# Kernel tuning notes

Measured on AMD Instinct MI355X. Metric: run time of the kernel, lower is better.

The kernel has to match this reference:

```python
import math
import jax, jax.numpy as jnp
import numpy as np

NUM_HEADS = 16
D_MODEL = 1024
D_HEAD = 64
D_SEQ = 2048
NUM_LAYERS = 24
BATCH = 2


def setup_inputs() -> dict:
    key = jax.random.key(0)
    ks = jax.random.split(key, 10)
    s = math.sqrt(0.02)
    residual = jax.random.normal(ks[0], (BATCH, D_SEQ, D_MODEL), dtype=jnp.float32)
    W_Q = jax.random.normal(ks[1], (NUM_HEADS, D_MODEL, D_HEAD), dtype=jnp.float32) * s
    W_K = jax.random.normal(ks[2], (NUM_HEADS, D_MODEL, D_HEAD), dtype=jnp.float32) * s
    W_V = jax.random.normal(ks[3], (NUM_HEADS, D_MODEL, D_HEAD), dtype=jnp.float32) * s
    W_O = jax.random.normal(ks[4], (NUM_HEADS * D_HEAD, D_MODEL), dtype=jnp.float32) * s
    W_O = W_O / math.sqrt(NUM_LAYERS)
    b_Q = jax.random.normal(ks[5], (NUM_HEADS, D_HEAD), dtype=jnp.float32) * s
    b_K = jax.random.normal(ks[6], (NUM_HEADS, D_HEAD), dtype=jnp.float32) * s
    b_V = jax.random.normal(ks[7], (NUM_HEADS, D_HEAD), dtype=jnp.float32) * s
    b_O = jax.random.normal(ks[8], (D_MODEL,), dtype=jnp.float32) * s
    return dict(residual=residual, W_Q=W_Q, W_K=W_K, W_V=W_V, W_O=W_O,
                b_Q=b_Q, b_K=b_K, b_V=b_V, b_O=b_O)


def reference(residual, W_Q, W_K, W_V, W_O, b_Q, b_K, b_V, b_O):
    # residual: [b, s, m]; W_{Q,K,V}: [h, m, d]; b_{Q,K,V}: [h, d]
    Q = jnp.einsum('hmd,bsm->bshd', W_Q, residual) + b_Q
    K = jnp.einsum('hmd,bsm->bshd', W_K, residual) + b_K
    V = jnp.einsum('hmd,bsm->bshd', W_V, residual) + b_V
    # full causal score matrix [b, h, s_q, s_k], masked with -inf above diagonal
    QK = jnp.einsum('bqhd,bkhd->bhqk', Q, K)
    seq = residual.shape[1]
    causal = jnp.triu(jnp.ones((seq, seq), dtype=bool), k=1)  # True above diag
    QK_masked = jnp.where(causal, -jnp.inf, QK)
    soft = jax.nn.softmax(QK_masked / math.sqrt(D_HEAD), axis=-1)
    attn = jnp.einsum('bhqk,bkhd->bqhd', soft, V)  # [b, s, h, d]
    multi_head = attn.reshape(attn.shape[0], attn.shape[1], NUM_HEADS * D_HEAD)
    return jnp.einsum('em,bqe->bqm', W_O, multi_head) + b_O
```

## Files before the change

kernel.cpp:

```cpp
#include <hip/hip_runtime.h>
#include <stdint.h>

typedef unsigned short u16;
typedef unsigned long long u64;
typedef _Float16 f16;
typedef __attribute__((ext_vector_type(8))) _Float16 f16x8;
typedef __attribute__((ext_vector_type(4))) float f32x4;
typedef __attribute__((ext_vector_type(16))) float f32x16;
typedef __attribute__((ext_vector_type(4))) unsigned short u16x4;
typedef __attribute__((ext_vector_type(8))) unsigned short u16x8;

#define NHEADS 16
#define DMODEL 1024
#define DHEAD 64
#define SEQ 2048
#define NBATCH 2
#define MROWS (NBATCH * SEQ)
#define NQKV 3072
#define SCQ 0.18033688011112042f

__device__ __forceinline__ u16 f2h(float x) {
  union { f16 h; u16 u; } v;
  v.h = (f16)x;
  return v.u;
}

__device__ __forceinline__ unsigned pk2u(float x, float y) {
  typedef __fp16 fp16x2 __attribute__((ext_vector_type(2)));
  fp16x2 h = __builtin_amdgcn_cvt_pkrtz(x, y);
  union { fp16x2 h; unsigned u; } v; v.h = h;
  return v.u;
}

__device__ __forceinline__ f16x8 mkfrag(unsigned w0, unsigned w1, unsigned w2, unsigned w3) {
  union { unsigned u[4]; f16x8 f; } t;
  t.u[0] = w0; t.u[1] = w1; t.u[2] = w2; t.u[3] = w3;
  return t.f;
}

__device__ __forceinline__ f16x8 vfrag(const char* row, int sz, int F, int hib8) {
  union { u64 u[2]; f16x8 f; } t;
  t.u[0] = *(const u64*)(row + (((2 * F) ^ sz) << 4) + hib8);
  t.u[1] = *(const u64*)(row + (((2 * F + 1) ^ sz) << 4) + hib8);
  return t.f;
}

__device__ __forceinline__ void gload_lds16(const void* g, void* l) {
  __builtin_amdgcn_global_load_lds(
      (const __attribute__((address_space(1))) void*)g,
      (__attribute__((address_space(3))) void*)l, 16, 0, 0);
}

__global__ __launch_bounds__(256) void prep_kernel(
    const float* __restrict__ X,
    const float* __restrict__ WQ, const float* __restrict__ WK,
    const float* __restrict__ WV, const float* __restrict__ WO,
    u16* __restrict__ Xh, u16* __restrict__ Wqkv, u16* __restrict__ Wo) {
  __shared__ u16 lt[64][72];
  int blk = blockIdx.x;
  if (blk < 2048) {
    int i = blk * 256 + threadIdx.x;
    const f32x4* xv = (const f32x4*)(X + (size_t)i * 8);
    f32x4 a = xv[0], b = xv[1];
    u16x8 o;
    o[0] = f2h(a[0]); o[1] = f2h(a[1]); o[2] = f2h(a[2]); o[3] = f2h(a[3]);
    o[4] = f2h(b[0]); o[5] = f2h(b[1]); o[6] = f2h(b[2]); o[7] = f2h(b[3]);
    *(u16x8*)(Xh + (size_t)i * 8) = o;
  } else if (blk < 2816) {
    int bb = blk - 2048;
    int mt = bb & 15, hh = (bb >> 4) & 15, qkv = bb >> 8;
    const float* W = (qkv == 0) ? WQ : (qkv == 1) ? WK : WV;
    int m_in = threadIdx.x >> 2, dq = threadIdx.x & 3;
    const f32x4* sp4 = (const f32x4*)(W + (size_t)hh * (DMODEL * DHEAD) +
                                      (size_t)(mt * 64 + m_in) * DHEAD + dq * 16);
#pragma unroll
    for (int v4 = 0; v4 < 4; ++v4) {
      f32x4 a = sp4[v4];
#pragma unroll
      for (int j = 0; j < 4; ++j) lt[dq * 16 + v4 * 4 + j][m_in] = f2h(a[j]);
    }
    __syncthreads();
    int d_in = threadIdx.x >> 2, mq = threadIdx.x & 3;
    size_t orow = ((size_t)(qkv * 1024 + hh * 64 + d_in)) * DMODEL + mt * 64 + mq * 16;
    u16x8 o0, o1;
#pragma unroll
    for (int j = 0; j < 8; ++j) {
      o0[j] = lt[d_in][mq * 16 + j];
      o1[j] = lt[d_in][mq * 16 + 8 + j];
    }
    *(u16x8*)(Wqkv + orow) = o0;
    *(u16x8*)(Wqkv + orow + 8) = o1;
  } else {
    int bb = blk - 2816;
    int mt = bb & 15, et = bb >> 4;
    int e_in = threadIdx.x >> 2, mq = threadIdx.x & 3;
    const f32x4* sp4 = (const f32x4*)(WO + (size_t)(et * 64 + e_in) * DMODEL + mt * 64 + mq * 16);
#pragma unroll
    for (int v4 = 0; v4 < 4; ++v4) {
      f32x4 a = sp4[v4];
#pragma unroll
      for (int j = 0; j < 4; ++j) lt[mq * 16 + v4 * 4 + j][e_in] = f2h(a[j]);
    }
    __syncthreads();
    int m_in = threadIdx.x >> 2, eq = threadIdx.x & 3;
    size_t orow = (size_t)(mt * 64 + m_in) * DMODEL + et * 64 + eq * 16;
    u16x8 o0, o1;
#pragma unroll
    for (int j = 0; j < 8; ++j) {
      o0[j] = lt[m_in][eq * 16 + j];
      o1[j] = lt[m_in][eq * 16 + 8 + j];
    }
    *(u16x8*)(Wo + orow) = o0;
    *(u16x8*)(Wo + orow + 8) = o1;
  }
}

__global__ __launch_bounds__(256, 2) void gemm_qkv(
    const u16* __restrict__ A, const u16* __restrict__ Bt,
    const float* __restrict__ bq, const float* __restrict__ bk, const float* __restrict__ bv,
    u16* __restrict__ Qo, u16* __restrict__ Ko, u16* __restrict__ Vto) {
  __shared__ u16 lds[2][8192];
  const int tid = threadIdx.x;
  const int wid = tid >> 6, lane = tid & 63, lr = lane & 15, lg = lane >> 4;
  const int wr = wid >> 1, wc = wid & 1;
  const int brow = blockIdx.y * 128, bcol = blockIdx.x * 128;

  f32x4 acc[4][4];
#pragma unroll
  for (int i = 0; i < 4; ++i)
#pragma unroll
    for (int j = 0; j < 4; ++j) acc[i][j] = (f32x4){0.f, 0.f, 0.f, 0.f};

#define STAGE(buf, kt)                                                               \
  {                                                                                  \
    _Pragma("unroll") for (int i = 0; i < 2; ++i) {                                  \
      int idx = tid + i * 256;                                                       \
      gload_lds16(A + (size_t)(brow + (idx >> 2)) * 1024 + (kt) * 32 + (idx & 3) * 8,\
                  (char*)&lds[buf][0] + (wid * 64 + i * 256) * 16);                  \
    }                                                                                \
    _Pragma("unroll") for (int i = 0; i < 2; ++i) {                                  \
      int idx = tid + i * 256;                                                       \
      gload_lds16(Bt + (size_t)(bcol + (idx >> 2)) * 1024 + (kt) * 32 + (idx & 3) * 8,\
                  (char*)&lds[buf][4096] + (wid * 64 + i * 256) * 16);               \
    }                                                                                \
  }

  STAGE(0, 0);
  __syncthreads();
  int cur = 0;
  for (int kt = 0; kt < 32; ++kt) {
    if (kt + 1 < 32) STAGE(cur ^ 1, kt + 1);
    const u16* Ab = &lds[cur][0];
    const u16* Bb = &lds[cur][4096];
    f16x8 a[4], b[4];
#pragma unroll
    for (int ar = 0; ar < 4; ++ar)
      a[ar] = *(const f16x8*)(Ab + (wr * 64 + ar * 16 + lr) * 32 + lg * 8);
#pragma unroll
    for (int bc = 0; bc < 4; ++bc)
      b[bc] = *(const f16x8*)(Bb + (wc * 64 + bc * 16 + lr) * 32 + lg * 8);
#pragma unroll
    for (int ar = 0; ar < 4; ++ar)
#pragma unroll
      for (int bc = 0; bc < 4; ++bc)
        acc[ar][bc] = __builtin_amdgcn_mfma_f32_16x16x32_f16(a[ar], b[bc], acc[ar][bc], 0, 0, 0);
    __syncthreads();
    cur ^= 1;
  }

#pragma unroll
  for (int ar = 0; ar < 4; ++ar) {
    int row0 = brow + wr * 64 + ar * 16 + lg * 4;
    int bb = row0 >> 11, s0 = row0 & 2047;
#pragma unroll
    for (int bc = 0; bc < 4; ++bc) {
      int n = bcol + wc * 64 + bc * 16 + lr;
      int qkv = n >> 10, hd = n & 1023, h = hd >> 6, d = hd & 63;
      float bias = ((qkv == 0) ? bq : (qkv == 1) ? bk : bv)[hd];
      if (qkv < 2) {
        u16* dst = qkv ? Ko : Qo;
        float sc = qkv ? 1.f : SCQ;
        size_t base = ((size_t)(bb * NHEADS + h) * SEQ + s0) * DHEAD + d;
#pragma unroll
        for (int r = 0; r < 4; ++r)
          dst[base + (size_t)r * DHEAD] = f2h((acc[ar][bc][r] + bias) * sc);
      } else {
        u16x4 o;
        o[0] = f2h(acc[ar][bc][0] + bias);
        o[1] = f2h(acc[ar][bc][1] + bias);
        o[2] = f2h(acc[ar][bc][2] + bias);
        o[3] = f2h(acc[ar][bc][3] + bias);
        *(u16x4*)(Vto + ((size_t)(bb * NHEADS + h) * DHEAD + d) * SEQ + s0) = o;
      }
    }
  }
}

__global__ __launch_bounds__(256, 2) void gemm_out(
    const u16* __restrict__ A, const u16* __restrict__ Bt,
    const float* __restrict__ bo, float* __restrict__ Co) {
  __shared__ u16 lds[2][8192];
  const int tid = threadIdx.x;
  const int wid = tid >> 6, lane = tid & 63, lr = lane & 15, lg = lane >> 4;
  const int wr = wid >> 1, wc = wid & 1;
  const int brow = blockIdx.y * 128, bcol = blockIdx.x * 128;

  f32x4 acc[4][4];
#pragma unroll
  for (int i = 0; i < 4; ++i)
#pragma unroll
    for (int j = 0; j < 4; ++j) acc[i][j] = (f32x4){0.f, 0.f, 0.f, 0.f};

  STAGE(0, 0);
  __syncthreads();
  int cur = 0;
  for (int kt = 0; kt < 32; ++kt) {
    if (kt + 1 < 32) STAGE(cur ^ 1, kt + 1);
    const u16* Ab = &lds[cur][0];
    const u16* Bb = &lds[cur][4096];
    f16x8 a[4], b[4];
#pragma unroll
    for (int ar = 0; ar < 4; ++ar)
      a[ar] = *(const f16x8*)(Ab + (wr * 64 + ar * 16 + lr) * 32 + lg * 8);
#pragma unroll
    for (int bc = 0; bc < 4; ++bc)
      b[bc] = *(const f16x8*)(Bb + (wc * 64 + bc * 16 + lr) * 32 + lg * 8);
#pragma unroll
    for (int ar = 0; ar < 4; ++ar)
#pragma unroll
      for (int bc = 0; bc < 4; ++bc)
        acc[ar][bc] = __builtin_amdgcn_mfma_f32_16x16x32_f16(a[ar], b[bc], acc[ar][bc], 0, 0, 0);
    __syncthreads();
    cur ^= 1;
  }
#undef STAGE

#pragma unroll
  for (int ar = 0; ar < 4; ++ar) {
    int row0 = brow + wr * 64 + ar * 16 + lg * 4;
#pragma unroll
    for (int bc = 0; bc < 4; ++bc) {
      int n = bcol + wc * 64 + bc * 16 + lr;
      float bias = bo[n];
#pragma unroll
      for (int r = 0; r < 4; ++r)
        Co[(size_t)(row0 + r) * DMODEL + n] = acc[ar][bc][r] + bias;
    }
  }
}

__global__ __launch_bounds__(128, 2) void attn_kernel(
    const u16* __restrict__ Q, const u16* __restrict__ K,
    const u16* __restrict__ Vt, u16* __restrict__ MH) {
  __shared__ char sh8[32768];
  const int tid = threadIdx.x, wid = tid >> 6, lane = tid & 63;
  const int l31 = lane & 31, hi = lane >> 5;
  const int bid = blockIdx.x;
  const int x = bid & 7, r = bid >> 3;
  const int bh = x + 8 * (r & 3);
  const int t = 31 - (r >> 2);
  const int h = bh & 15, b = bh >> 4;
  const u16* Qb = Q + (size_t)bh * (SEQ * DHEAD);
  const u16* Kb = K + (size_t)bh * (SEQ * DHEAD);
  const u16* Vb = Vt + (size_t)bh * (DHEAD * SEQ);

#pragma unroll
  for (int i = 0; i < 4; ++i) {
    int idx = tid + i * 128, row = idx >> 3;
    int sseg = (idx & 7) ^ ((row ^ (row >> 3)) & 7);
    gload_lds16(Qb + (size_t)(t * 64 + row) * DHEAD + sseg * 8, sh8 + 8192 + idx * 16);
    gload_lds16(Kb + (size_t)row * DHEAD + sseg * 8, sh8 + idx * 16);
    gload_lds16(Vb + (size_t)row * SEQ + sseg * 8, sh8 + 16384 + idx * 16);
  }
  __syncthreads();

  f16x8 qf0, qf1, qf2, qf3;
  {
    int row = (wid << 5) + l31;
    int swz = ((row ^ (row >> 3)) & 7) << 4;
    const char* qb = sh8 + 8192 + row * 128;
    qf0 = *(const f16x8*)(qb + ((hi * 16 + 0)  ^ swz));
    qf1 = *(const f16x8*)(qb + ((hi * 16 + 32) ^ swz));
    qf2 = *(const f16x8*)(qb + ((hi * 16 + 64) ^ swz));
    qf3 = *(const f16x8*)(qb + ((hi * 16 + 96) ^ swz));
  }
  __syncthreads();

  f32x16 acc0, acc1;
#pragma unroll
  for (int z = 0; z < 16; ++z) { acc0[z] = 0.f; acc1[z] = 0.f; }
  float m = -1e30f, l = 0.f;
  const int qa = t * 64 + (wid << 5) + l31;

  const int sw0 = (l31 ^ (l31 >> 3)) & 7;
  const int kz0 = sw0 << 4;
  const int r32 = 32 + l31;
  const int sw1 = (r32 ^ (r32 >> 3)) & 7;
  const int kz1 = sw1 << 4;
  const int hib = hi * 16;
  const int hib8 = hi * 8;

  for (int kt = 0; kt <= t; ++kt) {
    if (kt < t) {
      const int kb_n = ((kt + 1) & 1) ? 8192 : 0;
      const int vb_n = ((kt + 1) & 1) ? 24576 : 16384;
#pragma unroll
      for (int i = 0; i < 4; ++i) {
        int idx = tid + i * 128, rw = idx >> 3;
        int sseg = (idx & 7) ^ ((rw ^ (rw >> 3)) & 7);
        gload_lds16(Kb + (size_t)((kt + 1) * 64 + rw) * DHEAD + sseg * 8, sh8 + kb_n + idx * 16);
        gload_lds16(Vb + (size_t)rw * SEQ + (kt + 1) * 64 + sseg * 8, sh8 + vb_n + idx * 16);
      }
    }
    const char* kbuf = sh8 + ((kt & 1) ? 8192 : 0);
    const char* vbuf = sh8 + ((kt & 1) ? 24576 : 16384);

    f32x16 s0, s1;
#pragma unroll
    for (int z = 0; z < 16; ++z) { s0[z] = 0.f; s1[z] = 0.f; }
    {
      const char* kb0 = kbuf + l31 * 128;
      const char* kb1 = kbuf + r32 * 128;
      f16x8 kf;
      __builtin_amdgcn_s_setprio(1);
      kf = *(const f16x8*)(kb0 + ((hib + 0)  ^ kz0)); s0 = __builtin_amdgcn_mfma_f32_32x32x16_f16(kf, qf0, s0, 0, 0, 0);
      kf = *(const f16x8*)(kb0 + ((hib + 32) ^ kz0)); s0 = __builtin_amdgcn_mfma_f32_32x32x16_f16(kf, qf1, s0, 0, 0, 0);
      kf = *(const f16x8*)(kb0 + ((hib + 64) ^ kz0)); s0 = __builtin_amdgcn_mfma_f32_32x32x16_f16(kf, qf2, s0, 0, 0, 0);
      kf = *(const f16x8*)(kb0 + ((hib + 96) ^ kz0)); s0 = __builtin_amdgcn_mfma_f32_32x32x16_f16(kf, qf3, s0, 0, 0, 0);
      kf = *(const f16x8*)(kb1 + ((hib + 0)  ^ kz1)); s1 = __builtin_amdgcn_mfma_f32_32x32x16_f16(kf, qf0, s1, 0, 0, 0);
      kf = *(const f16x8*)(kb1 + ((hib + 32) ^ kz1)); s1 = __builtin_amdgcn_mfma_f32_32x32x16_f16(kf, qf1, s1, 0, 0, 0);
      kf = *(const f16x8*)(kb1 + ((hib + 64) ^ kz1)); s1 = __builtin_amdgcn_mfma_f32_32x32x16_f16(kf, qf2, s1, 0, 0, 0);
      kf = *(const f16x8*)(kb1 + ((hib + 96) ^ kz1)); s1 = __builtin_amdgcn_mfma_f32_32x32x16_f16(kf, qf3, s1, 0, 0, 0);
      __builtin_amdgcn_s_setprio(0);
    }

    if (kt == t) {
#pragma unroll
      for (int rr = 0; rr < 16; ++rr) {
        int k0 = kt * 64 + (rr & 3) + 8 * (rr >> 2) + 4 * hi;
        if (k0 > qa) s0[rr] = -1e30f;
        if (k0 + 32 > qa) s1[rr] = -1e30f;
      }
    }

    float tm = s0[0];
#pragma unroll
    for (int rr = 1; rr < 16; ++rr) tm = fmaxf(tm, s0[rr]);
#pragma unroll
    for (int rr = 0; rr < 16; ++rr) tm = fmaxf(tm, s1[rr]);
    tm = fmaxf(tm, __shfl_xor(tm, 32));

    if (!__all(tm <= m + 8.f)) {
      float m2 = fmaxf(m, tm);
      float al = exp2f(m - m2);
      m = m2;
      l *= al;
#pragma unroll
      for (int rr = 0; rr < 16; ++rr) {
        int qp = (rr & 3) + 8 * (rr >> 2) + 4 * hi;
        float af = __shfl(al, qp);
        acc0[rr] *= af;
        acc1[rr] *= af;
      }
    }

    float rs = 0.f;
#pragma unroll
    for (int rr = 0; rr < 16; ++rr) { s0[rr] = exp2f(s0[rr] - m); rs += s0[rr]; }
#pragma unroll
    for (int rr = 0; rr < 16; ++rr) { s1[rr] = exp2f(s1[rr] - m); rs += s1[rr]; }
    rs += __shfl_xor(rs, 32);
    l += rs;

    f16x8 pa0 = mkfrag(pk2u(s0[0],  s0[1]),  pk2u(s0[2],  s0[3]),
                       pk2u(s0[4],  s0[5]),  pk2u(s0[6],  s0[7]));
    f16x8 pa1 = mkfrag(pk2u(s0[8],  s0[9]),  pk2u(s0[10], s0[11]),
                       pk2u(s0[12], s0[13]), pk2u(s0[14], s0[15]));
    f16x8 pa2 = mkfrag(pk2u(s1[0],  s1[1]),  pk2u(s1[2],  s1[3]),
                       pk2u(s1[4],  s1[5]),  pk2u(s1[6],  s1[7]));
    f16x8 pa3 = mkfrag(pk2u(s1[8],  s1[9]),  pk2u(s1[10], s1[11]),
                       pk2u(s1[12], s1[13]), pk2u(s1[14], s1[15]));

    {
      const char* vr0 = vbuf + l31 * 128;
      const char* vr1 = vbuf + r32 * 128;
      __builtin_amdgcn_s_setprio(1);
      acc0 = __builtin_amdgcn_mfma_f32_32x32x16_f16(pa0, vfrag(vr0, sw0, 0, hib8), acc0, 0, 0, 0);
      acc0 = __builtin_amdgcn_mfma_f32_32x32x16_f16(pa1, vfrag(vr0, sw0, 1, hib8), acc0, 0, 0, 0);
      acc0 = __builtin_amdgcn_mfma_f32_32x32x16_f16(pa2, vfrag(vr0, sw0, 2, hib8), acc0, 0, 0, 0);
      acc0 = __builtin_amdgcn_mfma_f32_32x32x16_f16(pa3, vfrag(vr0, sw0, 3, hib8), acc0, 0, 0, 0);
      acc1 = __builtin_amdgcn_mfma_f32_32x32x16_f16(pa0, vfrag(vr1, sw1, 0, hib8), acc1, 0, 0, 0);
      acc1 = __builtin_amdgcn_mfma_f32_32x32x16_f16(pa1, vfrag(vr1, sw1, 1, hib8), acc1, 0, 0, 0);
      acc1 = __builtin_amdgcn_mfma_f32_32x32x16_f16(pa2, vfrag(vr1, sw1, 2, hib8), acc1, 0, 0, 0);
      acc1 = __builtin_amdgcn_mfma_f32_32x32x16_f16(pa3, vfrag(vr1, sw1, 3, hib8), acc1, 0, 0, 0);
      __builtin_amdgcn_s_setprio(0);
    }

    __syncthreads();
  }

#pragma unroll
  for (int rr = 0; rr < 16; ++rr) {
    int qp = (rr & 3) + 8 * (rr >> 2) + 4 * hi;
    float ls = __shfl(l, qp);
    int qrow = t * 64 + (wid << 5) + qp;
    size_t base = ((size_t)(b * SEQ) + qrow) * DMODEL + h * DHEAD;
    MH[base + l31]      = f2h(acc0[rr] / ls);
    MH[base + 32 + l31] = f2h(acc1[rr] / ls);
  }
}

extern "C" void kernel_launch(void* const* d_in, const int* in_sizes, int n_in,
                              void* d_out, int out_size, void* d_ws, size_t ws_size,
                              hipStream_t stream) {
  const float* residual = (const float*)d_in[0];
  const float* WQ = (const float*)d_in[1];
  const float* WK = (const float*)d_in[2];
  const float* WV = (const float*)d_in[3];
  const float* WO = (const float*)d_in[4];
  const float* bQ = (const float*)d_in[5];
  const float* bK = (const float*)d_in[6];
  const float* bV = (const float*)d_in[7];
  const float* bO = (const float*)d_in[8];
  float* out = (float*)d_out;

  char* w = (char*)d_ws;
  u16* Xh   = (u16*)(w);
  u16* Wqkv = (u16*)(w + ((size_t)8 << 20));
  u16* Wo   = (u16*)(w + ((size_t)14 << 20));
  u16* Qd   = (u16*)(w + ((size_t)16 << 20));
  u16* Kd   = (u16*)(w + ((size_t)24 << 20));
  u16* Vtd  = (u16*)(w + ((size_t)32 << 20));
  u16* MH   = (u16*)(w + ((size_t)40 << 20));

  prep_kernel<<<3072, 256, 0, stream>>>(residual, WQ, WK, WV, WO, Xh, Wqkv, Wo);

  gemm_qkv<<<dim3(NQKV / 128, MROWS / 128), 256, 0, stream>>>(
      Xh, Wqkv, bQ, bK, bV, Qd, Kd, Vtd);

  attn_kernel<<<1024, 128, 0, stream>>>(Qd, Kd, Vtd, MH);

  gemm_out<<<dim3(DMODEL / 128, MROWS / 128), 256, 0, stream>>>(MH, Wo, bO, out);
}
```

Measured before the change: 129.9 us.

## Widen attention blocks to 128 query rows sharing K/V tiles across four waves

The attention kernel now launches 512 blocks of 256 threads, and each block handles 128 query rows instead of 64. The four waves share each K/V tile loaded into LDS, which halves the global K/V traffic per query. Waves covering the lower query tile skip the last key tile and write their output early. Blocks are reordered so work is balanced between the two halves of the grid. The cost is idle waves on the final iteration and fewer blocks in flight, which may reduce latency hiding.

```diff
diff --git a/kernel.cpp b/kernel.cpp
--- a/kernel.cpp
+++ b/kernel.cpp
@@ -249,26 +249,36 @@
   }
 }
 
-__global__ __launch_bounds__(128, 2) void attn_kernel(
+__global__ __launch_bounds__(256, 2) void attn_kernel(
     const u16* __restrict__ Q, const u16* __restrict__ K,
     const u16* __restrict__ Vt, u16* __restrict__ MH) {
   __shared__ char sh8[32768];
   const int tid = threadIdx.x, wid = tid >> 6, lane = tid & 63;
   const int l31 = lane & 31, hi = lane >> 5;
   const int bid = blockIdx.x;
-  const int x = bid & 7, r = bid >> 3;
-  const int bh = x + 8 * (r & 3);
-  const int t = 31 - (r >> 2);
+  const int half = bid >> 8;
+  const int u = bid & 255;
+  const int jj = u >> 4;
+  const int j = half ? (15 - jj) : jj;
+  const int bh = (u & 15) + 16 * half;
   const int h = bh & 15, b = bh >> 4;
+  const int nt = 2 * j + 2;
+  const int tw = 2 * j + 1 + (wid >> 1);
   const u16* Qb = Q + (size_t)bh * (SEQ * DHEAD);
   const u16* Kb = K + (size_t)bh * (SEQ * DHEAD);
   const u16* Vb = Vt + (size_t)bh * (DHEAD * SEQ);
 
 #pragma unroll
   for (int i = 0; i < 4; ++i) {
-    int idx = tid + i * 128, row = idx >> 3;
+    int idx = tid + i * 256, row = idx >> 3;
     int sseg = (idx & 7) ^ ((row ^ (row >> 3)) & 7);
-    gload_lds16(Qb + (size_t)(t * 64 + row) * DHEAD + sseg * 8, sh8 + 8192 + idx * 16);
+    char* qdst = (idx < 512) ? sh8 + 8192 + idx * 16 : sh8 + 24576 + (idx - 512) * 16;
+    gload_lds16(Qb + (size_t)(128 * j + row) * DHEAD + sseg * 8, qdst);
+  }
+#pragma unroll
+  for (int i = 0; i < 2; ++i) {
+    int idx = tid + i * 256, row = idx >> 3;
+    int sseg = (idx & 7) ^ ((row ^ (row >> 3)) & 7);
     gload_lds16(Kb + (size_t)row * DHEAD + sseg * 8, sh8 + idx * 16);
     gload_lds16(Vb + (size_t)row * SEQ + sseg * 8, sh8 + 16384 + idx * 16);
   }
@@ -276,9 +286,9 @@
 
   f16x8 qf0, qf1, qf2, qf3;
   {
-    int row = (wid << 5) + l31;
+    int row = ((wid & 1) << 5) + l31;
     int swz = ((row ^ (row >> 3)) & 7) << 4;
-    const char* qb = sh8 + 8192 + row * 128;
+    const char* qb = sh8 + ((wid < 2) ? 8192 : 24576) + row * 128;
     qf0 = *(const f16x8*)(qb + ((hi * 16 + 0)  ^ swz));
     qf1 = *(const f16x8*)(qb + ((hi * 16 + 32) ^ swz));
     qf2 = *(const f16x8*)(qb + ((hi * 16 + 64) ^ swz));
@@ -290,7 +300,7 @@
 #pragma unroll
   for (int z = 0; z < 16; ++z) { acc0[z] = 0.f; acc1[z] = 0.f; }
   float m = -1e30f, l = 0.f;
-  const int qa = t * 64 + (wid << 5) + l31;
+  const int qa = 128 * j + (wid << 5) + l31;
 
   const int sw0 = (l31 ^ (l31 >> 3)) & 7;
   const int kz0 = sw0 << 4;
@@ -300,113 +310,120 @@
   const int hib = hi * 16;
   const int hib8 = hi * 8;
 
-  for (int kt = 0; kt <= t; ++kt) {
-    if (kt < t) {
+  for (int kt = 0; kt < nt; ++kt) {
+    if (kt + 1 < nt) {
       const int kb_n = ((kt + 1) & 1) ? 8192 : 0;
       const int vb_n = ((kt + 1) & 1) ? 24576 : 16384;
 #pragma unroll
-      for (int i = 0; i < 4; ++i) {
-        int idx = tid + i * 128, rw = idx >> 3;
+      for (int i = 0; i < 2; ++i) {
+        int idx = tid + i * 256, rw = idx >> 3;
         int sseg = (idx & 7) ^ ((rw ^ (rw >> 3)) & 7);
         gload_lds16(Kb + (size_t)((kt + 1) * 64 + rw) * DHEAD + sseg * 8, sh8 + kb_n + idx * 16);
         gload_lds16(Vb + (size_t)rw * SEQ + (kt + 1) * 64 + sseg * 8, sh8 + vb_n + idx * 16);
       }
     }
-    const char* kbuf = sh8 + ((kt & 1) ? 8192 : 0);
-    const char* vbuf = sh8 + ((kt & 1) ? 24576 : 16384);
-
-    f32x16 s0, s1;
-#pragma unroll
-    for (int z = 0; z < 16; ++z) { s0[z] = 0.f; s1[z] = 0.f; }
-    {
-      const char* kb0 = kbuf + l31 * 128;
-      const char* kb1 = kbuf + r32 * 128;
-      f16x8 kf;
-      __builtin_amdgcn_s_setprio(1);
-      kf = *(const f16x8*)(kb0 + ((hib + 0)  ^ kz0)); s0 = __builtin_amdgcn_mfma_f32_32x32x16_f16(kf, qf0, s0, 0, 0, 0);
-      kf = *(const f16x8*)(kb0 + ((hib + 32) ^ kz0)); s0 = __builtin_amdgcn_mfma_f32_32x32x16_f16(kf, qf1, s0, 0, 0, 0);
-      kf = *(const f16x8*)(kb0 + ((hib + 64) ^ kz0)); s0 = __builtin_amdgcn_mfma_f32_32x32x16_f16(kf, qf2, s0, 0, 0, 0);
-      kf = *(const f16x8*)(kb0 + ((hib + 96) ^ kz0)); s0 = __builtin_amdgcn_mfma_f32_32x32x16_f16(kf, qf3, s0, 0, 0, 0);
-      kf = *(const f16x8*)(kb1 + ((hib + 0)  ^ kz1)); s1 = __builtin_amdgcn_mfma_f32_32x32x16_f16(kf, qf0, s1, 0, 0, 0);
-      kf = *(const f16x8*)(kb1 + ((hib + 32) ^ kz1)); s1 = __builtin_amdgcn_mfma_f32_32x32x16_f16(kf, qf1, s1, 0, 0, 0);
-      kf = *(const f16x8*)(kb1 + ((hib + 64) ^ kz1)); s1 = __builtin_amdgcn_mfma_f32_32x32x16_f16(kf, qf2, s1, 0, 0, 0);
-      kf = *(const f16x8*)(kb1 + ((hib + 96) ^ kz1)); s1 = __builtin_amdgcn_mfma_f32_32x32x16_f16(kf, qf3, s1, 0, 0, 0);
-      __builtin_amdgcn_s_setprio(0);
-    }
-
-    if (kt == t) {
-#pragma unroll
-      for (int rr = 0; rr < 16; ++rr) {
-        int k0 = kt * 64 + (rr & 3) + 8 * (rr >> 2) + 4 * hi;
-        if (k0 > qa) s0[rr] = -1e30f;
-        if (k0 + 32 > qa) s1[rr] = -1e30f;
-      }
-    }
-
-    float tm = s0[0];
-#pragma unroll
-    for (int rr = 1; rr < 16; ++rr) tm = fmaxf(tm, s0[rr]);
-#pragma unroll
-    for (int rr = 0; rr < 16; ++rr) tm = fmaxf(tm, s1[rr]);
-    tm = fmaxf(tm, __shfl_xor(tm, 32));
-
-    if (!__all(tm <= m + 8.f)) {
-      float m2 = fmaxf(m, tm);
-      float al = exp2f(m - m2);
-      m = m2;
-      l *= al;
-#pragma unroll
-      for (int rr = 0; rr < 16; ++rr) {
-        int qp = (rr & 3) + 8 * (rr >> 2) + 4 * hi;
-        float af = __shfl(al, qp);
-        acc0[rr] *= af;
-        acc1[rr] *= af;
-      }
-    }
-
-    float rs = 0.f;
-#pragma unroll
-    for (int rr = 0; rr < 16; ++rr) { s0[rr] = exp2f(s0[rr] - m); rs += s0[rr]; }
-#pragma unroll
-    for (int rr = 0; rr < 16; ++rr) { s1[rr] = exp2f(s1[rr] - m); rs += s1[rr]; }
-    rs += __shfl_xor(rs, 32);
-    l += rs;
-
-    f16x8 pa0 = mkfrag(pk2u(s0[0],  s0[1]),  pk2u(s0[2],  s0[3]),
-                       pk2u(s0[4],  s0[5]),  pk2u(s0[6],  s0[7]));
-    f16x8 pa1 = mkfrag(pk2u(s0[8],  s0[9]),  pk2u(s0[10], s0[11]),
-                       pk2u(s0[12], s0[13]), pk2u(s0[14], s0[15]));
-    f16x8 pa2 = mkfrag(pk2u(s1[0],  s1[1]),  pk2u(s1[2],  s1[3]),
-                       pk2u(s1[4],  s1[5]),  pk2u(s1[6],  s1[7]));
-    f16x8 pa3 = mkfrag(pk2u(s1[8],  s1[9]),  pk2u(s1[10], s1[11]),
-                       pk2u(s1[12], s1[13]), pk2u(s1[14], s1[15]));
-
-    {
-      const char* vr0 = vbuf + l31 * 128;
-      const char* vr1 = vbuf + r32 * 128;
-      __builtin_amdgcn_s_setprio(1);
-      acc0 = __builtin_amdgcn_mfma_f32_32x32x16_f16(pa0, vfrag(vr0, sw0, 0, hib8), acc0, 0, 0, 0);
-      acc0 = __builtin_amdgcn_mfma_f32_32x32x16_f16(pa1, vfrag(vr0, sw0, 1, hib8), acc0, 0, 0, 0);
-      acc0 = __builtin_amdgcn_mfma_f32_32x32x16_f16(pa2, vfrag(vr0, sw0, 2, hib8), acc0, 0, 0, 0);
-      acc0 = __builtin_amdgcn_mfma_f32_32x32x16_f16(pa3, vfrag(vr0, sw0, 3, hib8), acc0, 0, 0, 0);
-      acc1 = __builtin_amdgcn_mfma_f32_32x32x16_f16(pa0, vfrag(vr1, sw1, 0, hib8), acc1, 0, 0, 0);
-      acc1 = __builtin_amdgcn_mfma_f32_32x32x16_f16(pa1, vfrag(vr1, sw1, 1, hib8), acc1, 0, 0, 0);
-      acc1 = __builtin_amdgcn_mfma_f32_32x32x16_f16(pa2, vfrag(vr1, sw1, 2, hib8), acc1, 0, 0, 0);
-      acc1 = __builtin_amdgcn_mfma_f32_32x32x16_f16(pa3, vfrag(vr1, sw1, 3, hib8), acc1, 0, 0, 0);
-      __builtin_amdgcn_s_setprio(0);
+    const bool act = (kt < tw);
+    const bool dg = (kt == tw - 1);
+
+    if (act) {
+      const char* kbuf = sh8 + ((kt & 1) ? 8192 : 0);
+      const char* vbuf = sh8 + ((kt & 1) ? 24576 : 16384);
+
+      f32x16 s0, s1;
+#pragma unroll
+      for (int z = 0; z < 16; ++z) { s0[z] = 0.f; s1[z] = 0.f; }
+      {
+        const char* kb0 = kbuf + l31 * 128;
+        const char* kb1 = kbuf + r32 * 128;
+        f16x8 kf;
+        __builtin_amdgcn_s_setprio(1);
+        kf = *(const f16x8*)(kb0 + ((hib + 0)  ^ kz0)); s0 = __builtin_amdgcn_mfma_f32_32x32x16_f16(kf, qf0, s0, 0, 0, 0);
+        kf = *(const f16x8*)(kb0 + ((hib + 32) ^ kz0)); s0 = __builtin_amdgcn_mfma_f32_32x32x16_f16(kf, qf1, s0, 0, 0, 0);
+        kf = *(const f16x8*)(kb0 + ((hib + 64) ^ kz0)); s0 = __builtin_amdgcn_mfma_f32_32x32x16_f16(kf, qf2, s0, 0, 0, 0);
+        kf = *(const f16x8*)(kb0 + ((hib + 96) ^ kz0)); s0 = __builtin_amdgcn_mfma_f32_32x32x16_f16(kf, qf3, s0, 0, 0, 0);
+        kf = *(const f16x8*)(kb1 + ((hib + 0)  ^ kz1)); s1 = __builtin_amdgcn_mfma_f32_32x32x16_f16(kf, qf0, s1, 0, 0, 0);
+        kf = *(const f16x8*)(kb1 + ((hib + 32) ^ kz1)); s1 = __builtin_amdgcn_mfma_f32_32x32x16_f16(kf, qf1, s1, 0, 0, 0);
+        kf = *(const f16x8*)(kb1 + ((hib + 64) ^ kz1)); s1 = __builtin_amdgcn_mfma_f32_32x32x16_f16(kf, qf2, s1, 0, 0, 0);
+        kf = *(const f16x8*)(kb1 + ((hib + 96) ^ kz1)); s1 = __builtin_amdgcn_mfma_f32_32x32x16_f16(kf, qf3, s1, 0, 0, 0);
+        __builtin_amdgcn_s_setprio(0);
+      }
+
+      if (dg) {
+#pragma unroll
+        for (int rr = 0; rr < 16; ++rr) {
+          int k0 = kt * 64 + (rr & 3) + 8 * (rr >> 2) + 4 * hi;
+          if (k0 > qa) s0[rr] = -1e30f;
+          if (k0 + 32 > qa) s1[rr] = -1e30f;
+        }
+      }
+
+      float tm = s0[0];
+#pragma unroll
+      for (int rr = 1; rr < 16; ++rr) tm = fmaxf(tm, s0[rr]);
+#pragma unroll
+      for (int rr = 0; rr < 16; ++rr) tm = fmaxf(tm, s1[rr]);
+      tm = fmaxf(tm, __shfl_xor(tm, 32));
+
+      if (!__all(tm <= m + 8.f)) {
+        float m2 = fmaxf(m, tm);
+        float al = exp2f(m - m2);
+        m = m2;
+        l *= al;
+#pragma unroll
+        for (int rr = 0; rr < 16; ++rr) {
+          int qp = (rr & 3) + 8 * (rr >> 2) + 4 * hi;
+          float af = __shfl(al, qp);
+          acc0[rr] *= af;
+          acc1[rr] *= af;
+        }
+      }
+
+      float rs = 0.f;
+#pragma unroll
+      for (int rr = 0; rr < 16; ++rr) { s0[rr] = exp2f(s0[rr] - m); rs += s0[rr]; }
+#pragma unroll
+      for (int rr = 0; rr < 16; ++rr) { s1[rr] = exp2f(s1[rr] - m); rs += s1[rr]; }
+      rs += __shfl_xor(rs, 32);
+      l += rs;
+
+      f16x8 pa0 = mkfrag(pk2u(s0[0],  s0[1]),  pk2u(s0[2],  s0[3]),
+                         pk2u(s0[4],  s0[5]),  pk2u(s0[6],  s0[7]));
+      f16x8 pa1 = mkfrag(pk2u(s0[8],  s0[9]),  pk2u(s0[10], s0[11]),
+                         pk2u(s0[12], s0[13]), pk2u(s0[14], s0[15]));
+      f16x8 pa2 = mkfrag(pk2u(s1[0],  s1[1]),  pk2u(s1[2],  s1[3]),
+                         pk2u(s1[4],  s1[5]),  pk2u(s1[6],  s1[7]));
+      f16x8 pa3 = mkfrag(pk2u(s1[8],  s1[9]),  pk2u(s1[10], s1[11]),
+                         pk2u(s1[12], s1[13]), pk2u(s1[14], s1[15]));
+
+      {
+        const char* vr0 = vbuf + l31 * 128;
+        const char* vr1 = vbuf + r32 * 128;
+        __builtin_amdgcn_s_setprio(1);
+        acc0 = __builtin_amdgcn_mfma_f32_32x32x16_f16(pa0, vfrag(vr0, sw0, 0, hib8), acc0, 0, 0, 0);
+        acc0 = __builtin_amdgcn_mfma_f32_32x32x16_f16(pa1, vfrag(vr0, sw0, 1, hib8), acc0, 0, 0, 0);
+        acc0 = __builtin_amdgcn_mfma_f32_32x32x16_f16(pa2, vfrag(vr0, sw0, 2, hib8), acc0, 0, 0, 0);
+        acc0 = __builtin_amdgcn_mfma_f32_32x32x16_f16(pa3, vfrag(vr0, sw0, 3, hib8), acc0, 0, 0, 0);
+        acc1 = __builtin_amdgcn_mfma_f32_32x32x16_f16(pa0, vfrag(vr1, sw1, 0, hib8), acc1, 0, 0, 0);
+        acc1 = __builtin_amdgcn_mfma_f32_32x32x16_f16(pa1, vfrag(vr1, sw1, 1, hib8), acc1, 0, 0, 0);
+        acc1 = __builtin_amdgcn_mfma_f32_32x32x16_f16(pa2, vfrag(vr1, sw1, 2, hib8), acc1, 0, 0, 0);
+        acc1 = __builtin_amdgcn_mfma_f32_32x32x16_f16(pa3, vfrag(vr1, sw1, 3, hib8), acc1, 0, 0, 0);
+        __builtin_amdgcn_s_setprio(0);
+      }
+
+      if (dg) {
+#pragma unroll
+        for (int rr = 0; rr < 16; ++rr) {
+          int qp = (rr & 3) + 8 * (rr >> 2) + 4 * hi;
+          float ls = __shfl(l, qp);
+          int qrow = 128 * j + (wid << 5) + qp;
+          size_t base = ((size_t)(b * SEQ) + qrow) * DMODEL + h * DHEAD;
+          MH[base + l31]      = f2h(acc0[rr] / ls);
+          MH[base + 32 + l31] = f2h(acc1[rr] / ls);
+        }
+      }
     }
 
     __syncthreads();
-  }
-
-#pragma unroll
-  for (int rr = 0; rr < 16; ++rr) {
-    int qp = (rr & 3) + 8 * (rr >> 2) + 4 * hi;
-    float ls = __shfl(l, qp);
-    int qrow = t * 64 + (wid << 5) + qp;
-    size_t base = ((size_t)(b * SEQ) + qrow) * DMODEL + h * DHEAD;
-    MH[base + l31]      = f2h(acc0[rr] / ls);
-    MH[base + 32 + l31] = f2h(acc1[rr] / ls);
   }
 }
 
@@ -438,7 +455,7 @@
   gemm_qkv<<<dim3(NQKV / 128, MROWS / 128), 256, 0, stream>>>(
       Xh, Wqkv, bQ, bK, bV, Qd, Kd, Vtd);
 
-  attn_kernel<<<1024, 128, 0, stream>>>(Qd, Kd, Vtd, MH);
+  attn_kernel<<<512, 256, 0, stream>>>(Qd, Kd, Vtd, MH);
 
   gemm_out<<<dim3(DMODEL / 128, MROWS / 128), 256, 0, stream>>>(MH, Wo, bO, out);
 }
```

Measured after the change: 125.1 us. 3.7% less time.
